# Kernel tuning notes

Hardware: AMD Instinct MI355X
Metric: run time of the kernel (lower is better)

Reference implementation:

```python
import jax, jax.numpy as jnp
import numpy as np

OUT = 7        # RoIAlign output_size
SR = 2         # sampling_ratio
SCALE = 1.0 / 32.0


def roi_align(feat, boxes):
    """Torchvision-style RoIAlign (aligned=False) for a single image.
    feat: [C,H,W]; boxes: [N,4] xyxy in image coords. Returns [N,C,OUT,OUT]."""
    C, H, W = feat.shape
    b = boxes * SCALE
    x1, y1, x2, y2 = b[:, 0], b[:, 1], b[:, 2], b[:, 3]
    rw = jnp.maximum(x2 - x1, 1.0)
    rh = jnp.maximum(y2 - y1, 1.0)
    bw = rw / OUT  # bin width
    bh = rh / OUT  # bin height
    P = OUT * SR   # 14 sample points per axis
    i = jnp.arange(P)
    bin_idx = (i // SR).astype(feat.dtype)
    sub_idx = (i % SR).astype(feat.dtype)
    # sample coords: start + bin*binsize + (s+0.5)*binsize/SR  -> [N,P]
    ox = x1[:, None] + bin_idx[None, :] * bw[:, None] + (sub_idx[None, :] + 0.5) * (bw[:, None] / SR)
    oy = y1[:, None] + bin_idx[None, :] * bh[:, None] + (sub_idx[None, :] + 0.5) * (bh[:, None] / SR)

    def axis_terms(o, L):
        valid = (o >= -1.0) & (o <= float(L))
        oc = jnp.clip(o, 0.0, L - 1.0)
        i0 = jnp.floor(oc).astype(jnp.int32)
        i1 = jnp.minimum(i0 + 1, L - 1)
        l = oc - i0.astype(oc.dtype)
        return valid, i0, i1, l

    vy, y0, y1i, ly = axis_terms(oy, H)
    vx, x0, x1i, lx = axis_terms(ox, W)
    valid = (vy[:, :, None] & vx[:, None, :]).astype(feat.dtype)  # [N,P,P]

    def gather(yi, xi):  # -> [C,N,P,P]
        return feat[:, yi[:, :, None], xi[:, None, :]]

    wy0, wy1 = (1.0 - ly), ly
    wx0, wx1 = (1.0 - lx), lx
    val = (gather(y0, x0) * (wy0[:, :, None] * wx0[:, None, :])
           + gather(y0, x1i) * (wy0[:, :, None] * wx1[:, None, :])
           + gather(y1i, x0) * (wy1[:, :, None] * wx0[:, None, :])
           + gather(y1i, x1i) * (wy1[:, :, None] * wx1[:, None, :]))
    val = val * valid[None]                      # zero out-of-bounds samples
    val = jnp.transpose(val, (1, 0, 2, 3))       # [N,C,P,P]
    N = boxes.shape[0]
    val = val.reshape(N, C, OUT, SR, OUT, SR)
    return val.mean(axis=(3, 5))                 # average sampling points


def reference(feats1, feats2, proposals, W1, b1, W2, b2):
    N = proposals.shape[0]
    f1 = roi_align(feats1[0], proposals).reshape(N, -1)  # [N, C*49]
    f2 = roi_align(feats2[0], proposals).reshape(N, -1)
    feats_cat = jnp.concatenate([f1, f2], axis=1)        # [N, 2*C*49]
    h = jax.nn.relu(feats_cat @ W1 + b1)
    out = h @ W2 + b2                                    # [N, 11]
    obj_scores = jax.nn.sigmoid(out[:, :2])
    boxes = out[:, 2:10].reshape(-1, 2, 4)
    id_scores = jax.nn.sigmoid(out[:, 10])
    return (obj_scores[:, 0], obj_scores[:, 1], boxes[:, 0], boxes[:, 1], id_scores)


def setup_inputs() -> dict:
    key = jax.random.key(0)
    ks = jax.random.split(key, 8)
    C, H, W = 256, 32, 32
    N = 1024
    IMG = 1024.0
    feats1 = jax.random.normal(ks[0], (1, C, H, W), dtype=jnp.float32)
    feats2 = jax.random.normal(ks[1], (1, C, H, W), dtype=jnp.float32)
    # valid xyxy boxes in image coords
    cx = jax.random.uniform(ks[2], (N,), minval=0.0, maxval=IMG)
    cy = jax.random.uniform(ks[3], (N,), minval=0.0, maxval=IMG)
    hw = jax.random.uniform(ks[4], (N, 2), minval=16.0, maxval=160.0)
    x1 = jnp.clip(cx - hw[:, 0], 0.0, IMG - 2.0)
    y1 = jnp.clip(cy - hw[:, 1], 0.0, IMG - 2.0)
    x2 = jnp.clip(cx + hw[:, 0], x1 + 1.0, IMG)
    y2 = jnp.clip(cy + hw[:, 1], y1 + 1.0, IMG)
    proposals = jnp.stack([x1, y1, x2, y2], axis=1).astype(jnp.float32)
    d_in = 2 * C * OUT * OUT  # 25088
    W1 = jax.random.normal(ks[5], (d_in, 512), dtype=jnp.float32) * 0.02
    b1 = jnp.zeros((512,), dtype=jnp.float32)
    W2 = jax.random.normal(ks[6], (512, 11), dtype=jnp.float32) * 0.02
    b2 = jnp.zeros((11,), dtype=jnp.float32)
    return {"feats1": feats1, "feats2": feats2, "proposals": proposals,
            "W1": W1, "b1": b1, "W2": W2, "b2": b2}
```

## Files before the change

### kernel.cpp

```cpp
#include <hip/hip_runtime.h>
#include <hip/hip_bf16.h>

#define KTOT   25088
#define HALF_K 12544
#define HID    512
#define SPLITK 14
#define KCHUNK (KTOT/SPLITK)
#define NTILE  28

typedef __attribute__((ext_vector_type(8))) short short8;
typedef __attribute__((ext_vector_type(4))) float f32x4;

__device__ __forceinline__ unsigned short f2bf(float x) {
  __hip_bfloat16 h = __float2bfloat16(x);
  return *reinterpret_cast<unsigned short*>(&h);
}
__device__ __forceinline__ float bf2f(unsigned short u) {
  return __uint_as_float((unsigned)u << 16);
}

__global__ __launch_bounds__(256) void k_tfeat(const float* __restrict__ f1,
                                               const float* __restrict__ f2,
                                               __hip_bfloat16* __restrict__ ft) {
  __shared__ float tile[64][65];
  const int ct = blockIdx.x, yxt = blockIdx.y, map = blockIdx.z;
  const float* src = map ? f2 : f1;
  const int t = threadIdx.x, t4 = t >> 6, tl = t & 63;
#pragma unroll
  for (int pass = 0; pass < 16; ++pass) {
    int cl = pass * 4 + t4;
    tile[cl][tl] = src[(ct * 64 + cl) * 1024 + yxt * 64 + tl];
  }
  __syncthreads();
#pragma unroll
  for (int pass = 0; pass < 16; ++pass) {
    int yl = pass * 4 + t4;
    ft[(size_t)map * 262144 + (size_t)(yxt * 64 + yl) * 256 + ct * 64 + tl] =
        __float2bfloat16(tile[tl][yl]);
  }
}

__global__ __launch_bounds__(256) void k_tw1(const float* __restrict__ W1,
                                             __hip_bfloat16* __restrict__ W1t) {
  __shared__ float tile[64][65];
  const int ct = blockIdx.x & 3, jt = blockIdx.x >> 2;
  const int p = blockIdx.y, map = blockIdx.z;
  const int t = threadIdx.x, t4 = t >> 6, tl = t & 63;
#pragma unroll
  for (int pass = 0; pass < 16; ++pass) {
    int cl = pass * 4 + t4;
    int c = ct * 64 + cl;
    size_t krow = (size_t)map * HALF_K + (size_t)c * 49 + p;
    tile[cl][tl] = W1[krow * HID + jt * 64 + tl];
  }
  __syncthreads();
#pragma unroll
  for (int pass = 0; pass < 16; ++pass) {
    int jl = pass * 4 + t4;
    int j = jt * 64 + jl;
    W1t[(size_t)j * KTOT + (size_t)map * HALF_K + p * 256 + ct * 64 + tl] =
        __float2bfloat16(tile[tl][jl]);
  }
}

__global__ __launch_bounds__(256) void k_roi(const __hip_bfloat16* __restrict__ ft,
                                             const float* __restrict__ props,
                                             __hip_bfloat16* __restrict__ A) {
  __shared__ int   s_ny[2];
  __shared__ int   s_yoff[2][4];
  __shared__ float s_wy[2][4];
  __shared__ int   s_nx[2][7];
  __shared__ int   s_xoff[2][7][4];
  __shared__ float s_wx[2][7][4];
  const int t = threadIdx.x;
  const int nb = blockIdx.x * 2;
  const int oy = blockIdx.y;
  const float sc = 1.0f / 32.0f;
  if (t < 16) {
    const int b = t & 1, j = t >> 1;
    const int n = nb + b;
    float bx1 = props[n * 4 + 0] * sc, by1 = props[n * 4 + 1] * sc;
    float bx2 = props[n * 4 + 2] * sc, by2 = props[n * 4 + 3] * sc;
    float bw = fmaxf(bx2 - bx1, 1.f) * (1.f / 7.f);
    float bh = fmaxf(by2 - by1, 1.f) * (1.f / 7.f);
    const bool isY = (j == 0);
    const int i = isY ? oy : (j - 1);
    const float start = isY ? by1 : bx1;
    const float bs = isY ? bh : bw;
    int idxs[4]; float ws[4];
#pragma unroll
    for (int ssub = 0; ssub < 2; ++ssub) {
      float o = start + (float)i * bs + ((float)ssub + 0.5f) * bs * 0.5f;
      float v = (o >= -1.f && o <= 32.f) ? 1.f : 0.f;
      float oc = fminf(fmaxf(o, 0.f), 31.f);
      int i0 = (int)oc;
      int i1 = min(i0 + 1, 31);
      float l = oc - (float)i0;
      idxs[ssub * 2 + 0] = i0; ws[ssub * 2 + 0] = v * (1.f - l);
      idxs[ssub * 2 + 1] = i1; ws[ssub * 2 + 1] = v * l;
    }
    int mi[4]; float mw[4]; int cnt = 0;
#pragma unroll
    for (int e = 0; e < 4; ++e) {
      if (ws[e] != 0.f) {
        bool found = false;
#pragma unroll
        for (int f = 0; f < 4; ++f)
          if (f < cnt && mi[f] == idxs[e]) { mw[f] += ws[e]; found = true; }
        if (!found) { mi[cnt] = idxs[e]; mw[cnt] = ws[e]; ++cnt; }
      }
    }
#pragma unroll
    for (int f = 0; f < 4; ++f) if (f >= cnt) { mi[f] = 0; mw[f] = 0.f; }
    if (isY) {
      s_ny[b] = cnt;
#pragma unroll
      for (int f = 0; f < 4; ++f) { s_yoff[b][f] = mi[f] * 16384; s_wy[b][f] = mw[f] * 0.25f; }
    } else {
      s_nx[b][j - 1] = cnt;
#pragma unroll
      for (int f = 0; f < 4; ++f) { s_xoff[b][j - 1][f] = mi[f] * 512; s_wx[b][j - 1][f] = mw[f]; }
    }
  }
  __syncthreads();
  const int b = t >> 7, map = (t >> 6) & 1, q = t & 63;
  const char* fb = (const char*)ft;
  const unsigned qoff = (unsigned)(map * 524288 + q * 8);
  const int n = nb + b;
  const int ny = s_ny[b];
  unsigned ybase[4]; float wyr[4];
#pragma unroll
  for (int yy = 0; yy < 4; ++yy) {
    ybase[yy] = qoff + (unsigned)s_yoff[b][yy];
    wyr[yy] = s_wy[b][yy];
  }
  __hip_bfloat16* outp = A + (size_t)n * KTOT + map * HALF_K + q * 4 + oy * 7 * 256;
  for (int bl = 0; bl < 7; ++bl) {
    const int nx = s_nx[b][bl];
    float a0 = 0.f, a1 = 0.f, a2 = 0.f, a3 = 0.f;
    for (int xx = 0; xx < nx; ++xx) {
      const unsigned xo = (unsigned)s_xoff[b][bl][xx];
      const float wxv = s_wx[b][bl][xx];
      for (int yy = 0; yy < ny; ++yy) {
        ushort4 u = *(const ushort4*)(fb + (ybase[yy] + xo));
        float w = wyr[yy] * wxv;
        a0 += w * bf2f(u.x); a1 += w * bf2f(u.y);
        a2 += w * bf2f(u.z); a3 += w * bf2f(u.w);
      }
    }
    ushort4 o;
    o.x = f2bf(a0); o.y = f2bf(a1); o.z = f2bf(a2); o.w = f2bf(a3);
    *(ushort4*)(outp + bl * 256) = o;
  }
}

__device__ __forceinline__ void gl_lds16(const __hip_bfloat16* g, __hip_bfloat16* l) {
  __builtin_amdgcn_global_load_lds((const __attribute__((address_space(1))) void*)g,
                                   (__attribute__((address_space(3))) void*)l, 16, 0, 0);
}

__global__ __launch_bounds__(256, 2) void k_gemm1(const __hip_bfloat16* __restrict__ A,
                                                  const __hip_bfloat16* __restrict__ Bt,
                                                  unsigned short* __restrict__ parts, int M) {
  __shared__ __align__(16) __hip_bfloat16 As[2][128 * 64];
  __shared__ __align__(16) __hip_bfloat16 Bs[2][128 * 64];
  const int t = threadIdx.x;
  const int bid = blockIdx.x;
  const int newid = (bid & 7) * 56 + (bid >> 3);
  const int tile = newid & 31, kc = newid >> 5;
  const int row0 = (tile >> 2) * 128, col0 = (tile & 3) * 128;
  const size_t k0 = (size_t)kc * KCHUNK;

  const int srow = t >> 3;
  const int sq = (t & 7) ^ (srow & 7);
  const __hip_bfloat16* ags = A  + (size_t)(row0 + srow) * KTOT + k0 + sq * 8;
  const __hip_bfloat16* bgs = Bt + (size_t)(col0 + srow) * KTOT + k0 + sq * 8;

  const int lane = t & 63, wid = t >> 6;
  const int wm = wid >> 1, wn = wid & 1;
  const int r = lane & 15, g = lane >> 4;
  const int qs0 = ((g ^ (r & 7)) * 16);
  const int qs1 = qs0 ^ 64;
  const char* aB = (const char*)&As[0][0] + (wm * 64 + r) * 128;
  const char* bB = (const char*)&Bs[0][0] + (wn * 64 + r) * 128;

  f32x4 acc[4][4];
#pragma unroll
  for (int m = 0; m < 4; ++m)
#pragma unroll
    for (int n = 0; n < 4; ++n) acc[m][n] = (f32x4){0.f, 0.f, 0.f, 0.f};

#define STAGE(KT, BUF) do {                                             \
    const __hip_bfloat16* a_ = ags + (size_t)(KT) * 64;                 \
    const __hip_bfloat16* b_ = bgs + (size_t)(KT) * 64;                 \
    _Pragma("unroll")                                                   \
    for (int i_ = 0; i_ < 4; ++i_) {                                    \
      gl_lds16(a_ + (size_t)i_ * 32 * KTOT, &As[BUF][t * 8 + i_ * 2048]); \
      gl_lds16(b_ + (size_t)i_ * 32 * KTOT, &Bs[BUF][t * 8 + i_ * 2048]); \
    } } while (0)

#define TILE(BUF) do { const int bo_ = (BUF) * 16384;                   \
    short8 a0[4], b0[4], a1[4], b1[4];                                  \
    _Pragma("unroll")                                                   \
    for (int m_ = 0; m_ < 4; ++m_) {                                    \
      a0[m_] = *(const short8*)(aB + bo_ + m_ * 2048 + qs0);            \
      b0[m_] = *(const short8*)(bB + bo_ + m_ * 2048 + qs0);            \
    }                                                                   \
    _Pragma("unroll")                                                   \
    for (int m_ = 0; m_ < 4; ++m_) {                                    \
      a1[m_] = *(const short8*)(aB + bo_ + m_ * 2048 + qs1);            \
      b1[m_] = *(const short8*)(bB + bo_ + m_ * 2048 + qs1);            \
    }                                                                   \
    asm volatile("s_waitcnt lgkmcnt(8)" ::: "memory");                  \
    __builtin_amdgcn_sched_barrier(0);                                  \
    __builtin_amdgcn_s_setprio(1);                                      \
    _Pragma("unroll")                                                   \
    for (int m_ = 0; m_ < 4; ++m_) { _Pragma("unroll")                  \
      for (int n_ = 0; n_ < 4; ++n_)                                    \
        acc[m_][n_] = __builtin_amdgcn_mfma_f32_16x16x32_bf16(          \
            a0[m_], b0[n_], acc[m_][n_], 0, 0, 0); }                    \
    __builtin_amdgcn_s_setprio(0);                                      \
    asm volatile("s_waitcnt lgkmcnt(0)" ::: "memory");                  \
    __builtin_amdgcn_sched_barrier(0);                                  \
    __builtin_amdgcn_s_setprio(1);                                      \
    _Pragma("unroll")                                                   \
    for (int m_ = 0; m_ < 4; ++m_) { _Pragma("unroll")                  \
      for (int n_ = 0; n_ < 4; ++n_)                                    \
        acc[m_][n_] = __builtin_amdgcn_mfma_f32_16x16x32_bf16(          \
            a1[m_], b1[n_], acc[m_][n_], 0, 0, 0); }                    \
    __builtin_amdgcn_s_setprio(0);                                      \
  } while (0)

#define SB0 __builtin_amdgcn_sched_barrier(0)

  STAGE(0, 0);
  STAGE(1, 1);
  for (int kt = 0; kt < NTILE - 1; ++kt) {
    asm volatile("s_waitcnt vmcnt(8)" ::: "memory"); SB0;
    __builtin_amdgcn_s_barrier(); SB0;
    TILE(kt & 1);
    SB0;
    if (kt < NTILE - 2) {
      __builtin_amdgcn_s_barrier(); SB0;
      STAGE(kt + 2, kt & 1);
    }
  }
  asm volatile("s_waitcnt vmcnt(0)" ::: "memory"); SB0;
  __builtin_amdgcn_s_barrier(); SB0;
  TILE(1);

#undef STAGE
#undef TILE
#undef SB0

  unsigned short* P = parts + (size_t)kc * ((size_t)M * HID);
#pragma unroll
  for (int m = 0; m < 4; ++m)
#pragma unroll
    for (int n = 0; n < 4; ++n)
#pragma unroll
      for (int q = 0; q < 4; ++q) {
        int rr = row0 + wm * 64 + m * 16 + g * 4 + q;
        int cc = col0 + wn * 64 + n * 16 + r;
        P[(size_t)rr * HID + cc] = f2bf(acc[m][n][q]);
      }
}

__global__ __launch_bounds__(256) void k_epi1(const unsigned short* __restrict__ parts,
                                              const float* __restrict__ b1,
                                              float* __restrict__ h, int M) {
  int idx = blockIdx.x * 256 + threadIdx.x;
  int row = idx >> 6;
  int cg = (idx & 63) * 8;
  const unsigned short* base = parts + (size_t)row * HID + cg;
  float a[8] = {0.f, 0.f, 0.f, 0.f, 0.f, 0.f, 0.f, 0.f};
  for (int p = 0; p < SPLITK; ++p) {
    short8 v = *(const short8*)(base + (size_t)p * ((size_t)M * HID));
#pragma unroll
    for (int e = 0; e < 8; ++e) a[e] += bf2f((unsigned short)v[e]);
  }
  float* ho = h + (size_t)row * HID + cg;
#pragma unroll
  for (int e = 0; e < 8; ++e) ho[e] = fmaxf(a[e] + b1[cg + e], 0.f);
}

__global__ __launch_bounds__(256) void k_head(const float* __restrict__ h,
                                              const float* __restrict__ W2,
                                              const float* __restrict__ b2,
                                              float* __restrict__ out, int N) {
  __shared__ float hrow[512];
  __shared__ float part[16][17];
  const int n = blockIdx.x, t = threadIdx.x;
  hrow[t]       = h[(size_t)n * HID + t];
  hrow[t + 256] = h[(size_t)n * HID + 256 + t];
  __syncthreads();
  int j = t & 15, kc = t >> 4;
  float a = 0.f;
  if (j < 11) {
#pragma unroll
    for (int kk = 0; kk < 32; ++kk) {
      int k = kc * 32 + kk;
      a += hrow[k] * W2[k * 11 + j];
    }
  }
  part[kc][j] = a;
  __syncthreads();
  if (t < 11) {
    float sm = b2[t];
#pragma unroll
    for (int k2 = 0; k2 < 16; ++k2) sm += part[k2][t];
    if (t == 0)      out[n] = 1.f / (1.f + expf(-sm));
    else if (t == 1) out[N + n] = 1.f / (1.f + expf(-sm));
    else if (t < 6)  out[2 * N + n * 4 + (t - 2)] = sm;
    else if (t < 10) out[6 * N + n * 4 + (t - 6)] = sm;
    else             out[10 * N + n] = 1.f / (1.f + expf(-sm));
  }
}

extern "C" void kernel_launch(void* const* d_in, const int* in_sizes, int n_in,
                              void* d_out, int out_size, void* d_ws, size_t ws_size,
                              hipStream_t stream) {
  const float* feats1 = (const float*)d_in[0];
  const float* feats2 = (const float*)d_in[1];
  const float* props  = (const float*)d_in[2];
  const float* W1     = (const float*)d_in[3];
  const float* b1     = (const float*)d_in[4];
  const float* W2     = (const float*)d_in[5];
  const float* b2     = (const float*)d_in[6];
  float* out = (float*)d_out;
  const int N = in_sizes[2] / 4;

  char* ws = (char*)d_ws;
  __hip_bfloat16* ft = (__hip_bfloat16*)ws;
  __hip_bfloat16* Abuf = (__hip_bfloat16*)(ws + (1u << 20));
  size_t offW1t = (1u << 20) + (size_t)N * KTOT * 2;
  __hip_bfloat16* W1t = (__hip_bfloat16*)(ws + offW1t);
  size_t offParts = offW1t + (size_t)HID * KTOT * 2;
  unsigned short* parts = (unsigned short*)(ws + offParts);
  size_t offH = offParts + (size_t)SPLITK * N * HID * 2;
  float* h = (float*)(ws + offH);

  k_tfeat<<<dim3(4, 16, 2), 256, 0, stream>>>(feats1, feats2, ft);
  k_tw1<<<dim3(32, 49, 2), 256, 0, stream>>>(W1, W1t);
  k_roi<<<dim3(N / 2, 7), 256, 0, stream>>>(ft, props, Abuf);
  k_gemm1<<<dim3(32 * SPLITK), 256, 0, stream>>>(Abuf, W1t, parts, N);
  k_epi1<<<dim3((N * HID) / 2048), 256, 0, stream>>>(parts, b1, h, N);
  k_head<<<dim3(N), 256, 0, stream>>>(h, W2, b2, out, N);
}
```

Measured before the change: 93.72 us.

## Widen RoI gather to 8 channels per thread and fuse split-K reduction into head

The RoI kernel now handles four boxes per block, and each thread loads and writes 8 bf16 channels (16 bytes) instead of 4. This halves the thread count per box and widens the memory accesses. Separately, the split-K partial-sum reduction, bias and ReLU move into the head kernel, which drops the separate epilogue launch and the round trip of the fp32 hidden buffer. The trade-off is that only 64 of 256 threads in the head kernel do the reduction, so that phase runs with less parallelism.

```diff
diff --git a/kernel.cpp b/kernel.cpp
--- a/kernel.cpp
+++ b/kernel.cpp
@@ -66,18 +66,18 @@
 __global__ __launch_bounds__(256) void k_roi(const __hip_bfloat16* __restrict__ ft,
                                              const float* __restrict__ props,
                                              __hip_bfloat16* __restrict__ A) {
-  __shared__ int   s_ny[2];
-  __shared__ int   s_yoff[2][4];
-  __shared__ float s_wy[2][4];
-  __shared__ int   s_nx[2][7];
-  __shared__ int   s_xoff[2][7][4];
-  __shared__ float s_wx[2][7][4];
+  __shared__ int   s_ny[4];
+  __shared__ int   s_yoff[4][4];
+  __shared__ float s_wy[4][4];
+  __shared__ int   s_nx[4][7];
+  __shared__ int   s_xoff[4][7][4];
+  __shared__ float s_wx[4][7][4];
   const int t = threadIdx.x;
-  const int nb = blockIdx.x * 2;
+  const int nb = blockIdx.x * 4;
   const int oy = blockIdx.y;
   const float sc = 1.0f / 32.0f;
-  if (t < 16) {
-    const int b = t & 1, j = t >> 1;
+  if (t < 32) {
+    const int b = t >> 3, j = t & 7;
     const int n = nb + b;
     float bx1 = props[n * 4 + 0] * sc, by1 = props[n * 4 + 1] * sc;
     float bx2 = props[n * 4 + 2] * sc, by2 = props[n * 4 + 3] * sc;
@@ -123,9 +123,9 @@
     }
   }
   __syncthreads();
-  const int b = t >> 7, map = (t >> 6) & 1, q = t & 63;
+  const int b = t >> 6, map = (t >> 5) & 1, q = t & 31;
   const char* fb = (const char*)ft;
-  const unsigned qoff = (unsigned)(map * 524288 + q * 8);
+  const unsigned qoff = (unsigned)(map * 524288 + q * 16);
   const int n = nb + b;
   const int ny = s_ny[b];
   unsigned ybase[4]; float wyr[4];
@@ -134,23 +134,24 @@
     ybase[yy] = qoff + (unsigned)s_yoff[b][yy];
     wyr[yy] = s_wy[b][yy];
   }
-  __hip_bfloat16* outp = A + (size_t)n * KTOT + map * HALF_K + q * 4 + oy * 7 * 256;
+  __hip_bfloat16* outp = A + (size_t)n * KTOT + map * HALF_K + q * 8 + oy * 7 * 256;
   for (int bl = 0; bl < 7; ++bl) {
     const int nx = s_nx[b][bl];
-    float a0 = 0.f, a1 = 0.f, a2 = 0.f, a3 = 0.f;
+    float a[8] = {0.f, 0.f, 0.f, 0.f, 0.f, 0.f, 0.f, 0.f};
     for (int xx = 0; xx < nx; ++xx) {
       const unsigned xo = (unsigned)s_xoff[b][bl][xx];
       const float wxv = s_wx[b][bl][xx];
       for (int yy = 0; yy < ny; ++yy) {
-        ushort4 u = *(const ushort4*)(fb + (ybase[yy] + xo));
+        short8 u = *(const short8*)(fb + (ybase[yy] + xo));
         float w = wyr[yy] * wxv;
-        a0 += w * bf2f(u.x); a1 += w * bf2f(u.y);
-        a2 += w * bf2f(u.z); a3 += w * bf2f(u.w);
+#pragma unroll
+        for (int e = 0; e < 8; ++e) a[e] += w * bf2f((unsigned short)u[e]);
       }
     }
-    ushort4 o;
-    o.x = f2bf(a0); o.y = f2bf(a1); o.z = f2bf(a2); o.w = f2bf(a3);
-    *(ushort4*)(outp + bl * 256) = o;
+    short8 o;
+#pragma unroll
+    for (int e = 0; e < 8; ++e) o[e] = (short)f2bf(a[e]);
+    *(short8*)(outp + bl * 256) = o;
   }
 }
 
@@ -266,33 +267,25 @@
       }
 }
 
-__global__ __launch_bounds__(256) void k_epi1(const unsigned short* __restrict__ parts,
+__global__ __launch_bounds__(256) void k_head(const unsigned short* __restrict__ parts,
                                               const float* __restrict__ b1,
-                                              float* __restrict__ h, int M) {
-  int idx = blockIdx.x * 256 + threadIdx.x;
-  int row = idx >> 6;
-  int cg = (idx & 63) * 8;
-  const unsigned short* base = parts + (size_t)row * HID + cg;
-  float a[8] = {0.f, 0.f, 0.f, 0.f, 0.f, 0.f, 0.f, 0.f};
-  for (int p = 0; p < SPLITK; ++p) {
-    short8 v = *(const short8*)(base + (size_t)p * ((size_t)M * HID));
-#pragma unroll
-    for (int e = 0; e < 8; ++e) a[e] += bf2f((unsigned short)v[e]);
-  }
-  float* ho = h + (size_t)row * HID + cg;
-#pragma unroll
-  for (int e = 0; e < 8; ++e) ho[e] = fmaxf(a[e] + b1[cg + e], 0.f);
-}
-
-__global__ __launch_bounds__(256) void k_head(const float* __restrict__ h,
                                               const float* __restrict__ W2,
                                               const float* __restrict__ b2,
                                               float* __restrict__ out, int N) {
   __shared__ float hrow[512];
   __shared__ float part[16][17];
   const int n = blockIdx.x, t = threadIdx.x;
-  hrow[t]       = h[(size_t)n * HID + t];
-  hrow[t + 256] = h[(size_t)n * HID + 256 + t];
+  if (t < 64) {
+    float a[8] = {0.f, 0.f, 0.f, 0.f, 0.f, 0.f, 0.f, 0.f};
+    const unsigned short* base = parts + (size_t)n * HID + t * 8;
+    for (int p = 0; p < SPLITK; ++p) {
+      short8 v = *(const short8*)(base + (size_t)p * ((size_t)N * HID));
+#pragma unroll
+      for (int e = 0; e < 8; ++e) a[e] += bf2f((unsigned short)v[e]);
+    }
+#pragma unroll
+    for (int e = 0; e < 8; ++e) hrow[t * 8 + e] = fmaxf(a[e] + b1[t * 8 + e], 0.f);
+  }
   __syncthreads();
   int j = t & 15, kc = t >> 4;
   float a = 0.f;
@@ -337,13 +330,10 @@
   __hip_bfloat16* W1t = (__hip_bfloat16*)(ws + offW1t);
   size_t offParts = offW1t + (size_t)HID * KTOT * 2;
   unsigned short* parts = (unsigned short*)(ws + offParts);
-  size_t offH = offParts + (size_t)SPLITK * N * HID * 2;
-  float* h = (float*)(ws + offH);
 
   k_tfeat<<<dim3(4, 16, 2), 256, 0, stream>>>(feats1, feats2, ft);
   k_tw1<<<dim3(32, 49, 2), 256, 0, stream>>>(W1, W1t);
-  k_roi<<<dim3(N / 2, 7), 256, 0, stream>>>(ft, props, Abuf);
+  k_roi<<<dim3(N / 4, 7), 256, 0, stream>>>(ft, props, Abuf);
   k_gemm1<<<dim3(32 * SPLITK), 256, 0, stream>>>(Abuf, W1t, parts, N);
-  k_epi1<<<dim3((N * HID) / 2048), 256, 0, stream>>>(parts, b1, h, N);
-  k_head<<<dim3(N), 256, 0, stream>>>(h, W2, b2, out, N);
-}
+  k_head<<<dim3(N), 256, 0, stream>>>(parts, b1, W2, b2, out, N);
+}
```

Result: faster. 83.01 us (-11.4%).
